# Kernel tuning notes

Measured on AMD Instinct MI355X. Metric: run time of the kernel, lower is better.

Reference implementation:

```python
import jax, jax.numpy as jnp
import numpy as np

B_, N, C, H, WS, NW = 2048, 49, 384, 12, 7, 64
D = C // H  # head_dim = 32
SCALE = D ** -0.5


def _relative_position_index(ws=WS):
    coords = np.stack(np.meshgrid(np.arange(ws), np.arange(ws), indexing='ij'))  # [2,ws,ws]
    flat = coords.reshape(2, -1)                         # [2, N]
    rel = flat[:, :, None] - flat[:, None, :]            # [2, N, N]
    rel = rel.transpose(1, 2, 0)                         # [N, N, 2]
    rel[..., 0] += ws - 1
    rel[..., 1] += ws - 1
    rel[..., 0] *= 2 * ws - 1
    return rel.sum(-1).astype(np.int32)                  # [N, N]


def setup_inputs() -> dict:
    key = jax.random.key(0)
    ks = jax.random.split(key, 9)
    return {
        'x1': jax.random.normal(ks[0], (B_, N, C), jnp.float32),
        'x2': jax.random.normal(ks[1], (B_, N, C), jnp.float32),
        'mask1': jax.random.normal(ks[2], (NW, N, N), jnp.float32),
        'mask2': jax.random.normal(ks[3], (NW, N, N), jnp.float32),
        'w_qkv': jax.random.normal(ks[4], (C, 3 * C), jnp.float32) * 0.02,
        'b_qkv': jax.random.normal(ks[5], (3 * C,), jnp.float32) * 0.02,
        'w_proj': jax.random.normal(ks[6], (C, C), jnp.float32) * 0.02,
        'b_proj': jax.random.normal(ks[7], (C,), jnp.float32) * 0.02,
        'rpb_table': jax.random.normal(ks[8], ((2 * WS - 1) ** 2, H), jnp.float32) * 0.02,
        'rel_index': jnp.asarray(_relative_position_index()),
    }


def _qkv(x, w_qkv, b_qkv):
    # x: [B_, N, C] -> q,k,v each [B_, H, N, D]
    qkv = (x @ w_qkv + b_qkv).reshape(B_, N, 3, H, D).transpose(2, 0, 3, 1, 4)
    return qkv[0], qkv[1], qkv[2]


def reference(x1, x2, mask1, mask2, w_qkv, b_qkv, w_proj, b_proj, rpb_table, rel_index):
    # relative position bias: [H, N, N]
    rpb = rpb_table[rel_index.reshape(-1)].reshape(N, N, H).transpose(2, 0, 1)

    q1, k1, v1 = _qkv(x1, w_qkv, b_qkv)
    _, k2, v2 = _qkv(x2, w_qkv, b_qkv)
    q1s = q1 * SCALE

    attn1 = jnp.einsum('bhnd,bhmd->bhnm', q1s, k1) + rpb[None]
    attn2 = jnp.einsum('bhnd,bhmd->bhnm', q1s, k2) + rpb[None]  # note: q1, per source

    # shifted-window mask add: [B_//nW, nW, H, N, N] + mask[None, :, None]
    attn1 = (attn1.reshape(B_ // NW, NW, H, N, N) + mask1[None, :, None]).reshape(B_, H, N, N)
    attn2 = (attn2.reshape(B_ // NW, NW, H, N, N) + mask2[None, :, None]).reshape(B_, H, N, N)

    attn = jax.nn.softmax(jnp.concatenate([attn1, attn2], axis=1), axis=-1)  # [B_, 2H, N, N]

    v = jnp.concatenate([v1, v2], axis=1)  # [B_, 2H, N, D]
    out = jnp.einsum('bhnm,bhmd->bhnd', attn, v)
    weights = out.transpose(0, 2, 1, 3).reshape(B_, N, 2 * C)
    x = weights[:, :, :C] @ w_proj + b_proj
    return x, weights
```

## Files before the change

### kernel.cpp

```cpp
#include <hip/hip_runtime.h>

typedef unsigned short u16;
typedef unsigned int u32;
typedef __attribute__((ext_vector_type(8))) short short8;
typedef __attribute__((ext_vector_type(4))) float f32x4;

#define NB 2048
#define NTOK 49
#define CH 384
#define NH 12
#define HD 32
#define SCALE_Q 0.17677669529663687f
#define TABF 1956864

__device__ __forceinline__ u16 f2bf(float f) {
  u32 u = __float_as_uint(f);
  u += 0x7fffu + ((u >> 16) & 1u);
  return (u16)(u >> 16);
}
__device__ __forceinline__ float bf2f(u16 h) { return __uint_as_float(((u32)h) << 16); }
__device__ __forceinline__ u32 pk2(float a, float b) { return (u32)f2bf(a) | ((u32)f2bf(b) << 16); }

__device__ __forceinline__ void gload16(const u16* g, u16* l) {
  __builtin_amdgcn_global_load_lds(
      (const __attribute__((address_space(1))) u32*)g,
      (__attribute__((address_space(3))) u32*)l,
      16, 0, 0);
}

__global__ void prep_w(const float* __restrict__ w_qkv, const float* __restrict__ w_proj,
                       u16* __restrict__ wqkvT, u16* __restrict__ wprojT)
{
  int idx = blockIdx.x * 256 + threadIdx.x;
  if (idx < 1152 * 384) {
    int n = idx / 384, k = idx - n * 384;
    wqkvT[idx] = f2bf(w_qkv[(size_t)k * 1152 + n]);
  } else if (idx < 1152 * 384 + 384 * 384) {
    int i2 = idx - 1152 * 384;
    int n = i2 / 384, k = i2 - n * 384;
    wprojT[i2] = f2bf(w_proj[(size_t)k * 384 + n]);
  }
}

__global__ __launch_bounds__(256) void prep_c(const float* __restrict__ rpb_table,
                                              const int* __restrict__ rel_index,
                                              const float* __restrict__ mask1,
                                              const float* __restrict__ mask2,
                                              float* __restrict__ comb)
{
  const int wbh = blockIdx.x;
  const int wb = wbh / 12, h = wbh - wb * 12;
  const size_t ob = (size_t)wbh * (49 * 52);
  for (int r = threadIdx.x; r < 2401; r += 256) {
    int i = r / 49, j = r - i * 49;
    float rv = rpb_table[(size_t)rel_index[r] * 12 + h];
    comb[ob + i * 52 + j]        = rv + mask1[(size_t)wb * 2401 + r];
    comb[TABF + ob + i * 52 + j] = rv + mask2[(size_t)wb * 2401 + r];
  }
}

__global__ __launch_bounds__(256) void conv_bf16(const float* __restrict__ x1, const float* __restrict__ x2,
                                                 u16* __restrict__ xb1, u16* __restrict__ xb2)
{
  const size_t i = ((size_t)blockIdx.x * 256 + threadIdx.x) * 8;
  float4 a = *reinterpret_cast<const float4*>(x1 + i);
  float4 b = *reinterpret_cast<const float4*>(x1 + i + 4);
  uint4 o;
  o.x = pk2(a.x, a.y); o.y = pk2(a.z, a.w); o.z = pk2(b.x, b.y); o.w = pk2(b.z, b.w);
  *reinterpret_cast<uint4*>(xb1 + i) = o;
  a = *reinterpret_cast<const float4*>(x2 + i);
  b = *reinterpret_cast<const float4*>(x2 + i + 4);
  o.x = pk2(a.x, a.y); o.y = pk2(a.z, a.w); o.z = pk2(b.x, b.y); o.w = pk2(b.z, b.w);
  *reinterpret_cast<uint4*>(xb2 + i) = o;
}

__global__ __launch_bounds__(256) void gemm_qkv(
    const u16* __restrict__ xb1, const u16* __restrict__ xb2,
    const u16* __restrict__ wT, const float* __restrict__ bias,
    u16* __restrict__ q1, u16* __restrict__ k1, u16* __restrict__ v1,
    u16* __restrict__ k2, u16* __restrict__ v2)
{
  __shared__ __align__(16) u16 smem[19456];
  u16* Cs = smem;

  const int bid0 = blockIdx.x;
  const int lin = (bid0 & 7) * 1470 + (bid0 >> 3);
  const int mt = lin / 15;
  const int nt = lin - mt * 15;

  const bool isx2 = nt >= 9;
  const u16* __restrict__ X = isx2 ? xb2 : xb1;
  const int colbase = isx2 ? 384 + (nt - 9) * 128 : nt * 128;
  const int m0 = mt * 128;
  const int tid = threadIdx.x;
  const int lane = tid & 63, wv = tid >> 6;
  const int wr = wv >> 1, wc = wv & 1;
  const int l15 = lane & 15, l4 = lane >> 4;

  f32x4 acc[4][4] = {};

  const u16* ga = X + (size_t)(m0 + l15) * CH + l4 * 8;
  const u16* gb = wT + (size_t)(colbase + l15) * CH + l4 * 8;
  const int g0 = wv, g1 = wv + 4;
  const int go0 = g0 * 16 * CH, go1 = g1 * 16 * CH;

  auto stage = [&](int bs, int kk) {
    u16* A = smem + bs * 8192;
    u16* B = A + 4096;
    gload16(ga + kk + go0, A + g0 * 512);
    gload16(gb + kk + go0, B + g0 * 512);
    gload16(ga + kk + go1, A + g1 * 512);
    gload16(gb + kk + go1, B + g1 * 512);
  };

  stage(0, 0);
  stage(1, 32);

#pragma unroll
  for (int k = 0; k < 12; ++k) {
    if (k < 11) asm volatile("s_waitcnt vmcnt(4)" ::: "memory");
    else        asm volatile("s_waitcnt vmcnt(0)" ::: "memory");
    __builtin_amdgcn_s_barrier();
    __builtin_amdgcn_sched_barrier(0);
    const int cb = k & 1;
    const u16* A = smem + cb * 8192;
    const u16* B = A + 4096;
    short8 af[4], bfr[4];
#pragma unroll
    for (int i = 0; i < 4; ++i)
      af[i] = *reinterpret_cast<const short8*>(&A[(wr * 4 + i) * 512 + lane * 8]);
#pragma unroll
    for (int j = 0; j < 4; ++j)
      bfr[j] = *reinterpret_cast<const short8*>(&B[(wc * 4 + j) * 512 + lane * 8]);
#pragma unroll
    for (int i = 0; i < 4; ++i)
#pragma unroll
      for (int j = 0; j < 4; ++j)
        acc[i][j] = __builtin_amdgcn_mfma_f32_16x16x32_bf16(af[i], bfr[j], acc[i][j], 0, 0, 0);
    asm volatile("s_waitcnt lgkmcnt(0)" ::: "memory");
    __builtin_amdgcn_s_barrier();
    __builtin_amdgcn_sched_barrier(0);
    if (k + 2 < 12) stage(cb, (k + 2) * 32);
  }

#pragma unroll
  for (int j = 0; j < 4; ++j) {
    const int colL = wc * 64 + j * 16 + l15;
    const int gcol = colbase + colL;
    const float bb = bias[gcol];
    const float scl = (gcol < 384) ? SCALE_Q : 1.0f;
#pragma unroll
    for (int i = 0; i < 4; ++i)
#pragma unroll
      for (int r = 0; r < 4; ++r) {
        const int row = wr * 64 + i * 16 + l4 * 4 + r;
        Cs[row * 152 + (colL ^ (((row >> 2) & 3) << 3))] = f2bf((acc[i][j][r] + bb) * scl);
      }
  }
  __syncthreads();

  u16* dst;
  int tb;
  if (colbase < 384)      { dst = q1;              tb = colbase; }
  else if (colbase < 768) { dst = isx2 ? k2 : k1;  tb = colbase - 384; }
  else                    { dst = isx2 ? v2 : v1;  tb = colbase - 768; }

#pragma unroll
  for (int u = 0; u < 8; ++u) {
    const int pc = tid + u * 256;
    const int row = pc >> 4, pp = pc & 15;
    const uint4 val = *reinterpret_cast<const uint4*>(&Cs[row * 152 + ((pp ^ ((row >> 2) & 3)) << 3)]);
    const int gm = m0 + row;
    const int b = gm / 49, tok = gm - b * 49;
    const int cm = tb + pp * 8;
    const int h = cm >> 5, d0 = cm & 31;
    *reinterpret_cast<uint4*>(&dst[(((size_t)b * NH + h) * NTOK + tok) * HD + d0]) = val;
  }
}

__global__ __launch_bounds__(256) void attn_kernel(
    const u16* __restrict__ q1, const u16* __restrict__ k1, const u16* __restrict__ v1,
    const u16* __restrict__ k2, const u16* __restrict__ v2,
    const float* __restrict__ comb, float* __restrict__ outw)
{
  __shared__ __align__(16) u16 VT[2][32][72];
  __shared__ __align__(16) u16 Pb[4][2][512];

  const int h = blockIdx.x, b = blockIdx.y;
  const int tid = threadIdx.x;
  const int lane = tid & 63, wt = tid >> 6;
  const int l15 = lane & 15, l4 = lane >> 4;
  const size_t base = ((size_t)b * NH + h) * 1568;

  for (int e = tid; e < 392; e += 256) {
    const int p = e >= 196;
    const int e2 = e - p * 196;
    const int tok = e2 >> 2, d8 = (e2 & 3) * 8;
    const u16* src = (p ? v2 : v1) + base + tok * 32 + d8;
    uint4 val = *reinterpret_cast<const uint4*>(src);
    const u16* pv = reinterpret_cast<const u16*>(&val);
#pragma unroll
    for (int q = 0; q < 8; ++q) VT[p][d8 + q][tok] = pv[q];
  }
  for (int e = tid; e < 2 * 32 * 15; e += 256) {
    int p = (e >= 480) ? 1 : 0;
    int e2 = e - p * 480;
    int d = e2 / 15, j = 49 + (e2 - d * 15);
    VT[p][d][j] = 0;
  }

  const short8 aq = *reinterpret_cast<const short8*>(&q1[base + (wt * 16 + l15) * 32 + l4 * 8]);

  __syncthreads();

  const int wb = b & 63;
  const int irow = wt * 16 + l15;
  const float* cb0 = comb + ((size_t)(wb * 12 + h) * 49 + (irow < 49 ? irow : 48)) * 52;
  const size_t obase = (size_t)b * (NTOK * 768) + (size_t)h * 32;

#pragma unroll
  for (int p = 0; p < 2; ++p) {
    const u16* __restrict__ kp = p ? k2 : k1;
    const float* cbp = cb0 + (size_t)p * TABF;

    f32x4 st[4];
    __builtin_amdgcn_s_setprio(1);
#pragma unroll
    for (int jt = 0; jt < 4; ++jt) {
      short8 bk = *reinterpret_cast<const short8*>(&kp[base + (jt * 16 + l15) * 32 + l4 * 8]);
      st[jt] = __builtin_amdgcn_mfma_f32_16x16x32_bf16(bk, aq, (f32x4){0.f, 0.f, 0.f, 0.f}, 0, 0, 0);
    }
    __builtin_amdgcn_s_setprio(0);

#pragma unroll
    for (int jt = 0; jt < 4; ++jt) {
      const float4 c = *reinterpret_cast<const float4*>(cbp + jt * 16 + l4 * 4);
#pragma unroll
      for (int r = 0; r < 4; ++r) {
        const int j = jt * 16 + l4 * 4 + r;
        st[jt][r] = (j < 49) ? st[jt][r] + (&c.x)[r] : -1e30f;
      }
    }

    float mx = -1e30f;
#pragma unroll
    for (int jt = 0; jt < 4; ++jt)
#pragma unroll
      for (int r = 0; r < 4; ++r) mx = fmaxf(mx, st[jt][r]);
    mx = fmaxf(mx, __shfl_xor(mx, 16));
    mx = fmaxf(mx, __shfl_xor(mx, 32));
    float sm = 0.f;
#pragma unroll
    for (int jt = 0; jt < 4; ++jt)
#pragma unroll
      for (int r = 0; r < 4; ++r) {
        float e = __expf(st[jt][r] - mx);
        st[jt][r] = e;
        sm += e;
      }
    sm += __shfl_xor(sm, 16);
    sm += __shfl_xor(sm, 32);
    const float si = 1.f / sm;

#pragma unroll
    for (int jt = 0; jt < 4; ++jt) {
      const int kt = jt >> 1;
#pragma unroll
      for (int r = 0; r < 4; r += 2) {
        const u32 pkv = pk2(st[jt][r] * si, st[jt][r + 1] * si);
        const int jrel = (jt & 1) * 16 + l4 * 4 + r;
        const int off = ((jrel >> 3) << 7) + l15 * 8 + (jrel & 7);
        *reinterpret_cast<u32*>(&Pb[wt][kt][off]) = pkv;
      }
    }

    f32x4 o[2] = {};
    __builtin_amdgcn_s_setprio(1);
#pragma unroll
    for (int kt = 0; kt < 2; ++kt) {
      short8 ap = *reinterpret_cast<const short8*>(&Pb[wt][kt][lane * 8]);
#pragma unroll
      for (int n2 = 0; n2 < 2; ++n2) {
        short8 bvf = *reinterpret_cast<const short8*>(&VT[p][n2 * 16 + l15][kt * 32 + l4 * 8]);
        o[n2] = __builtin_amdgcn_mfma_f32_16x16x32_bf16(ap, bvf, o[n2], 0, 0, 0);
      }
    }
    __builtin_amdgcn_s_setprio(0);

#pragma unroll
    for (int n2 = 0; n2 < 2; ++n2)
#pragma unroll
      for (int r = 0; r < 4; ++r) {
        const int i = wt * 16 + l4 * 4 + r;
        if (i < 49)
          outw[obase + (size_t)i * 768 + p * 384 + n2 * 16 + l15] = o[n2][r];
      }
  }
}

__global__ __launch_bounds__(256) void gemm_proj(
    const float* __restrict__ Wsrc, const u16* __restrict__ wT,
    const float* __restrict__ bias, float* __restrict__ outx)
{
  __shared__ __align__(16) u16 smem[16384];
  const int bid0 = blockIdx.x;
  const int lin = (bid0 & 7) * 294 + (bid0 >> 3);
  const int mt = lin / 3;
  const int nt = lin - mt * 3;

  const int colbase = nt * 128;
  const int m0 = mt * 128;
  const int tid = threadIdx.x;
  const int lane = tid & 63, wv = tid >> 6;
  const int wr = wv >> 1, wc = wv & 1;
  const int l15 = lane & 15, l4 = lane >> 4;

  f32x4 acc[4][4] = {};

  const float* ga = Wsrc + (size_t)(m0 + l15) * 768 + l4 * 8;
  const u16*   gb = wT + (size_t)(colbase + l15) * CH + l4 * 8;
  const int g0 = wv, g1 = wv + 4;

  float4 ar0[2][2], ar1[2][2];
  auto loadA = [&](float4 (*ar)[2], int kk) {
    ar[0][0] = *reinterpret_cast<const float4*>(ga + kk + g0 * 16 * 768);
    ar[0][1] = *reinterpret_cast<const float4*>(ga + kk + g0 * 16 * 768 + 4);
    ar[1][0] = *reinterpret_cast<const float4*>(ga + kk + g1 * 16 * 768);
    ar[1][1] = *reinterpret_cast<const float4*>(ga + kk + g1 * 16 * 768 + 4);
  };
  auto stageB = [&](int bs, int kk) {
    u16* B = smem + bs * 8192 + 4096;
    gload16(gb + kk + g0 * 16 * CH, B + g0 * 512);
    gload16(gb + kk + g1 * 16 * CH, B + g1 * 512);
  };
  auto writeA = [&](float4 (*ar)[2], int bs) {
    u16* A = smem + bs * 8192;
    uint4 v;
    v.x = pk2(ar[0][0].x, ar[0][0].y); v.y = pk2(ar[0][0].z, ar[0][0].w);
    v.z = pk2(ar[0][1].x, ar[0][1].y); v.w = pk2(ar[0][1].z, ar[0][1].w);
    *reinterpret_cast<uint4*>(&A[g0 * 512 + lane * 8]) = v;
    v.x = pk2(ar[1][0].x, ar[1][0].y); v.y = pk2(ar[1][0].z, ar[1][0].w);
    v.z = pk2(ar[1][1].x, ar[1][1].y); v.w = pk2(ar[1][1].z, ar[1][1].w);
    *reinterpret_cast<uint4*>(&A[g1 * 512 + lane * 8]) = v;
  };

  loadA(ar0, 0);  stageB(0, 0);
  loadA(ar1, 32); stageB(1, 32);

#pragma unroll
  for (int k = 0; k < 12; ++k) {
    if (k < 11) asm volatile("s_waitcnt vmcnt(6)" ::: "memory");
    else        asm volatile("s_waitcnt vmcnt(0)" ::: "memory");
    const int cb = k & 1;
    if (cb == 0) writeA(ar0, 0); else writeA(ar1, 1);
    asm volatile("s_waitcnt lgkmcnt(0)" ::: "memory");
    __builtin_amdgcn_s_barrier();
    __builtin_amdgcn_sched_barrier(0);
    const u16* A = smem + cb * 8192;
    const u16* B = A + 4096;
    short8 af[4], bfr[4];
#pragma unroll
    for (int i = 0; i < 4; ++i)
      af[i] = *reinterpret_cast<const short8*>(&A[(wr * 4 + i) * 512 + lane * 8]);
#pragma unroll
    for (int j = 0; j < 4; ++j)
      bfr[j] = *reinterpret_cast<const short8*>(&B[(wc * 4 + j) * 512 + lane * 8]);
#pragma unroll
    for (int i = 0; i < 4; ++i)
#pragma unroll
      for (int j = 0; j < 4; ++j)
        acc[i][j] = __builtin_amdgcn_mfma_f32_16x16x32_bf16(af[i], bfr[j], acc[i][j], 0, 0, 0);
    asm volatile("s_waitcnt lgkmcnt(0)" ::: "memory");
    __builtin_amdgcn_s_barrier();
    __builtin_amdgcn_sched_barrier(0);
    if (k + 2 < 12) {
      if (cb == 0) loadA(ar0, (k + 2) * 32); else loadA(ar1, (k + 2) * 32);
      stageB(cb, (k + 2) * 32);
    }
  }

#pragma unroll
  for (int j = 0; j < 4; ++j) {
    const int col = colbase + wc * 64 + j * 16 + l15;
    const float bb = bias[col];
#pragma unroll
    for (int i = 0; i < 4; ++i) {
#pragma unroll
      for (int r = 0; r < 4; ++r) {
        const int gm = m0 + wr * 64 + i * 16 + l4 * 4 + r;
        outx[(size_t)gm * CH + col] = acc[i][j][r] + bb;
      }
    }
  }
}

extern "C" void kernel_launch(void* const* d_in, const int* in_sizes, int n_in,
                              void* d_out, int out_size, void* d_ws, size_t ws_size,
                              hipStream_t stream) {
  const float* x1        = (const float*)d_in[0];
  const float* x2        = (const float*)d_in[1];
  const float* mask1     = (const float*)d_in[2];
  const float* mask2     = (const float*)d_in[3];
  const float* w_qkv     = (const float*)d_in[4];
  const float* b_qkv     = (const float*)d_in[5];
  const float* w_proj    = (const float*)d_in[6];
  const float* b_proj    = (const float*)d_in[7];
  const float* rpb_table = (const float*)d_in[8];
  const int*   rel_index = (const int*)d_in[9];

  float* outx = (float*)d_out;
  const size_t SZe = (size_t)NB * NH * NTOK * HD;
  float* outw = outx + SZe;

  u16* q1 = (u16*)d_out;
  u16* k1 = q1 + SZe;
  u16* xb1 = (u16*)outw;
  u16* xb2 = xb1 + SZe;

  u16* v1 = (u16*)d_ws;
  u16* k2 = v1 + SZe;
  u16* v2 = k2 + SZe;
  u16* wqkvT  = v2 + SZe;
  u16* wprojT = wqkvT + 1152 * 384;
  float* comb = (float*)(wprojT + 384 * 384);

  prep_w<<<2304, 256, 0, stream>>>(w_qkv, w_proj, wqkvT, wprojT);
  prep_c<<<768, 256, 0, stream>>>(rpb_table, rel_index, mask1, mask2, comb);
  conv_bf16<<<(int)(SZe / (256 * 8)), 256, 0, stream>>>(x1, x2, xb1, xb2);
  gemm_qkv<<<11760, 256, 0, stream>>>(xb1, xb2, wqkvT, b_qkv, q1, k1, v1, k2, v2);
  attn_kernel<<<dim3(12, 2048), 256, 0, stream>>>(q1, k1, v1, k2, v2, comb, outw);
  gemm_proj<<<2352, 256, 0, stream>>>(outw, wprojT, b_proj, outx);
}
```

Before: 748.3 us.

## Keep full QKV weight tile in LDS and stream activations through registers

The QKV GEMM now uses 512-thread blocks with 256x128 output tiles. The whole 128x384 weight slice is loaded into LDS once, and activation fragments are read straight from global memory into a three-deep register prefetch ring. This removes the per-k-step LDS double-buffer staging and its two barriers per iteration, and doubles the rows that reuse each weight tile. The cost is a 96KB LDS footprint that limits blocks per CU, plus global A loads whose latency the register prefetch has to hide.

```diff
diff --git a/kernel.cpp b/kernel.cpp
--- a/kernel.cpp
+++ b/kernel.cpp
@@ -74,78 +74,74 @@
   *reinterpret_cast<uint4*>(xb2 + i) = o;
 }
 
-__global__ __launch_bounds__(256) void gemm_qkv(
+__global__ __launch_bounds__(512, 2) void gemm_qkv(
     const u16* __restrict__ xb1, const u16* __restrict__ xb2,
     const u16* __restrict__ wT, const float* __restrict__ bias,
     u16* __restrict__ q1, u16* __restrict__ k1, u16* __restrict__ v1,
     u16* __restrict__ k2, u16* __restrict__ v2)
 {
-  __shared__ __align__(16) u16 smem[19456];
-  u16* Cs = smem;
+  __shared__ __align__(16) u16 Bs[49152];
 
   const int bid0 = blockIdx.x;
-  const int lin = (bid0 & 7) * 1470 + (bid0 >> 3);
+  const int lin = (bid0 & 7) * 735 + (bid0 >> 3);
   const int mt = lin / 15;
   const int nt = lin - mt * 15;
 
   const bool isx2 = nt >= 9;
   const u16* __restrict__ X = isx2 ? xb2 : xb1;
   const int colbase = isx2 ? 384 + (nt - 9) * 128 : nt * 128;
-  const int m0 = mt * 128;
+  const int m0 = mt * 256;
   const int tid = threadIdx.x;
-  const int lane = tid & 63, wv = tid >> 6;
-  const int wr = wv >> 1, wc = wv & 1;
+  const int lane = tid & 63, w = tid >> 6;
+  const int wm = w & 3, wn = w >> 2;
   const int l15 = lane & 15, l4 = lane >> 4;
 
+  {
+    const u16* gbw = wT + (size_t)(colbase + w * 16 + l15) * CH + l4 * 8;
+#pragma unroll
+    for (int u = 0; u < 12; ++u)
+      gload16(gbw + u * 32, &Bs[(w * 12 + u) * 512]);
+  }
+  __builtin_amdgcn_sched_barrier(0);
+
+  const u16* gaw = X + (size_t)(m0 + wm * 64 + l15) * CH + l4 * 8;
+  short8 areg[3][4];
+#pragma unroll
+  for (int pk = 0; pk < 3; ++pk)
+#pragma unroll
+    for (int i = 0; i < 4; ++i)
+      areg[pk][i] = *reinterpret_cast<const short8*>(gaw + i * 16 * CH + pk * 32);
+
+  asm volatile("s_waitcnt vmcnt(12)" ::: "memory");
+  __builtin_amdgcn_s_barrier();
+  __builtin_amdgcn_sched_barrier(0);
+
   f32x4 acc[4][4] = {};
-
-  const u16* ga = X + (size_t)(m0 + l15) * CH + l4 * 8;
-  const u16* gb = wT + (size_t)(colbase + l15) * CH + l4 * 8;
-  const int g0 = wv, g1 = wv + 4;
-  const int go0 = g0 * 16 * CH, go1 = g1 * 16 * CH;
-
-  auto stage = [&](int bs, int kk) {
-    u16* A = smem + bs * 8192;
-    u16* B = A + 4096;
-    gload16(ga + kk + go0, A + g0 * 512);
-    gload16(gb + kk + go0, B + g0 * 512);
-    gload16(ga + kk + go1, A + g1 * 512);
-    gload16(gb + kk + go1, B + g1 * 512);
-  };
-
-  stage(0, 0);
-  stage(1, 32);
-
-#pragma unroll
-  for (int k = 0; k < 12; ++k) {
-    if (k < 11) asm volatile("s_waitcnt vmcnt(4)" ::: "memory");
-    else        asm volatile("s_waitcnt vmcnt(0)" ::: "memory");
-    __builtin_amdgcn_s_barrier();
-    __builtin_amdgcn_sched_barrier(0);
-    const int cb = k & 1;
-    const u16* A = smem + cb * 8192;
-    const u16* B = A + 4096;
-    short8 af[4], bfr[4];
+#pragma unroll
+  for (int ks = 0; ks < 12; ++ks) {
+    short8 bfr[4];
+#pragma unroll
+    for (int j = 0; j < 4; ++j)
+      bfr[j] = *reinterpret_cast<const short8*>(&Bs[((wn * 4 + j) * 12 + ks) * 512 + lane * 8]);
 #pragma unroll
     for (int i = 0; i < 4; ++i)
-      af[i] = *reinterpret_cast<const short8*>(&A[(wr * 4 + i) * 512 + lane * 8]);
-#pragma unroll
-    for (int j = 0; j < 4; ++j)
-      bfr[j] = *reinterpret_cast<const short8*>(&B[(wc * 4 + j) * 512 + lane * 8]);
-#pragma unroll
-    for (int i = 0; i < 4; ++i)
 #pragma unroll
       for (int j = 0; j < 4; ++j)
-        acc[i][j] = __builtin_amdgcn_mfma_f32_16x16x32_bf16(af[i], bfr[j], acc[i][j], 0, 0, 0);
-    asm volatile("s_waitcnt lgkmcnt(0)" ::: "memory");
-    __builtin_amdgcn_s_barrier();
-    __builtin_amdgcn_sched_barrier(0);
-    if (k + 2 < 12) stage(cb, (k + 2) * 32);
-  }
+        acc[i][j] = __builtin_amdgcn_mfma_f32_16x16x32_bf16(areg[ks % 3][i], bfr[j], acc[i][j], 0, 0, 0);
+    if (ks + 3 < 12) {
+#pragma unroll
+      for (int i = 0; i < 4; ++i)
+        areg[ks % 3][i] = *reinterpret_cast<const short8*>(gaw + i * 16 * CH + (ks + 3) * 32);
+    }
+  }
+
+  asm volatile("s_waitcnt lgkmcnt(0)" ::: "memory");
+  __builtin_amdgcn_s_barrier();
+  u16* Cs = Bs;
 
 #pragma unroll
   for (int j = 0; j < 4; ++j) {
-    const int colL = wc * 64 + j * 16 + l15;
+    const int colL = wn * 64 + j * 16 + l15;
     const int gcol = colbase + colL;
     const float bb = bias[gcol];
     const float scl = (gcol < 384) ? SCALE_Q : 1.0f;
@@ -153,7 +149,7 @@
     for (int i = 0; i < 4; ++i)
 #pragma unroll
       for (int r = 0; r < 4; ++r) {
-        const int row = wr * 64 + i * 16 + l4 * 4 + r;
+        const int row = wm * 64 + i * 16 + l4 * 4 + r;
         Cs[row * 152 + (colL ^ (((row >> 2) & 3) << 3))] = f2bf((acc[i][j][r] + bb) * scl);
       }
   }
@@ -167,7 +163,7 @@
 
 #pragma unroll
   for (int u = 0; u < 8; ++u) {
-    const int pc = tid + u * 256;
+    const int pc = tid + u * 512;
     const int row = pc >> 4, pp = pc & 15;
     const uint4 val = *reinterpret_cast<const uint4*>(&Cs[row * 152 + ((pp ^ ((row >> 2) & 3)) << 3)]);
     const int gm = m0 + row;
@@ -427,7 +423,7 @@
   prep_w<<<2304, 256, 0, stream>>>(w_qkv, w_proj, wqkvT, wprojT);
   prep_c<<<768, 256, 0, stream>>>(rpb_table, rel_index, mask1, mask2, comb);
   conv_bf16<<<(int)(SZe / (256 * 8)), 256, 0, stream>>>(x1, x2, xb1, xb2);
-  gemm_qkv<<<11760, 256, 0, stream>>>(xb1, xb2, wqkvT, b_qkv, q1, k1, v1, k2, v2);
+  gemm_qkv<<<5880, 512, 0, stream>>>(xb1, xb2, wqkvT, b_qkv, q1, k1, v1, k2, v2);
   attn_kernel<<<dim3(12, 2048), 256, 0, stream>>>(q1, k1, v1, k2, v2, comb, outw);
   gemm_proj<<<2352, 256, 0, stream>>>(outw, wprojT, b_proj, outx);
 }
```

Result: slower. 817.6 us (+9.3%).
